# Performance work log

Hardware: AMD Instinct MI355X
Metric: run time of the kernel (lower is better)

Reference implementation:

```python
import jax, jax.numpy as jnp
import numpy as np

EMBED_DIM = 1024
SCALE = 1.0 / float(np.sqrt(EMBED_DIM))


def setup_inputs() -> dict:
    key = jax.random.key(0)
    ks = jax.random.split(key, 7)
    B, S, D = 4, 2048, EMBED_DIM
    init = 1.0 / np.sqrt(D)
    x = jax.random.normal(ks[0], (B, S, D), dtype=jnp.float32)
    Wq = jax.random.uniform(ks[1], (D, D), jnp.float32, -init, init)
    bq = jax.random.uniform(ks[2], (D,), jnp.float32, -init, init)
    Wk = jax.random.uniform(ks[3], (D, D), jnp.float32, -init, init)
    bk = jax.random.uniform(ks[4], (D,), jnp.float32, -init, init)
    Wv = jax.random.uniform(ks[5], (D, D), jnp.float32, -init, init)
    bv = jax.random.uniform(ks[6], (D,), jnp.float32, -init, init)
    return {"x": x, "Wq": Wq, "bq": bq, "Wk": Wk, "bk": bk, "Wv": Wv, "bv": bv}


def reference(x, Wq, bq, Wk, bk, Wv, bv):
    # Linear projections (torch Linear: x @ W.T + b; here W stored as [in, out])
    q = x @ Wq + bq  # [B, S, D]
    k = x @ Wk + bk
    v = x @ Wv + bv
    # Manual scaled dot-product attention (single head)
    scores = jnp.einsum("bsd,btd->bst", q, k) * SCALE  # [B, S, S]
    attn = jax.nn.softmax(scores, axis=-1)
    # Dropout is identity at inference (eval mode); p=0.1 at train time.
    return jnp.einsum("bst,btd->bsd", attn, v)
```

## Files before the change

### kernel.cpp

```cpp
#include <hip/hip_runtime.h>

#define MODE_QKV 0
#define MODE_S   1
#define MODE_PV  2

typedef __attribute__((ext_vector_type(8))) short short8;
typedef __attribute__((ext_vector_type(4))) float floatx4;

typedef const unsigned __attribute__((address_space(1)))* gp_t;
typedef unsigned __attribute__((address_space(3)))* lp_t;

__device__ __forceinline__ void async16(const void* g, void* l) {
  __builtin_amdgcn_global_load_lds((gp_t)g, (lp_t)l, 16, 0, 0);
}

__device__ __forceinline__ unsigned short f2bf(float f) {
  union { float f; unsigned u; } x; x.f = f;
  unsigned r = x.u + 0x7fffu + ((x.u >> 16) & 1u);
  return (unsigned short)(r >> 16);
}
__device__ __forceinline__ float bf2f(unsigned short h) {
  union { unsigned u; float f; } x; x.u = ((unsigned)h) << 16;
  return x.f;
}

union SmemU {
  struct { unsigned short A[2][4096]; unsigned short B[2][4096]; } st;
  unsigned short epi[128 * 136];
};

template<int MODE>
__global__ __launch_bounds__(256, 4)
void gemm_nt(const unsigned short* __restrict__ A,
             const unsigned short* __restrict__ Bmat,
             const float* __restrict__ b0, const float* __restrict__ b1,
             const float* __restrict__ b2,
             unsigned short* __restrict__ O0, unsigned short* __restrict__ O1,
             unsigned short* __restrict__ O2,
             float* __restrict__ Of, float* __restrict__ lsum,
             int M, int N, int K, long aZ, long bZ, long cZ, float scale)
{
  __shared__ SmemU smem;

  const int tid = threadIdx.x;
  const int wave = tid >> 6, lane = tid & 63;
  const int wm = wave >> 1, wn = wave & 1;
  const int quad = lane >> 4, l16 = lane & 15;

  const int gx = gridDim.x, gy = gridDim.y;
  int z, bm, bn;
  {
    int f = (blockIdx.z * gy + blockIdx.y) * gx + blockIdx.x;
    int T = gx * gy * (int)gridDim.z;
    int nsq = T >> 7;
    int xcd = f & 7, i = f >> 3;
    int sq = xcd * nsq + (i >> 4);
    int w = i & 15;
    int spz = (gx >> 2) * (gy >> 2);
    z = sq / spz;
    int sqr = sq - z * spz;
    int sqm = sqr / (gx >> 2), sqn = sqr - sqm * (gx >> 2);
    bm = (sqm * 4 + (w >> 2)) * 128;
    bn = (sqn * 4 + (w & 3)) * 128;
  }

  const unsigned short* Ap = (MODE == MODE_QKV) ? A : (A + (long)z * aZ);
  const unsigned short* Bp = Bmat + (long)z * bZ;

  floatx4 acc[4][4];
  #pragma unroll
  for (int i = 0; i < 4; i++)
    #pragma unroll
    for (int j = 0; j < 4; j++)
      acc[i][j] = (floatx4){0.f, 0.f, 0.f, 0.f};

  char* asb = (char*)&smem.st.A[0][0] + wave * 1024;
  char* bsb = (char*)&smem.st.B[0][0] + wave * 1024;

  for (int k0 = 0; k0 < K; k0 += 64) {
    #pragma unroll
    for (int p = 0; p < 2; p++) {
      #pragma unroll
      for (int h = 0; h < 2; h++) {
        int flat = tid + h * 256;
        int r = flat >> 2, c = (flat & 3) << 3;
        async16(Ap + (long)(bm + r) * K + k0 + p * 32 + c,
                asb + p * 8192 + h * 4096);
        async16(Bp + (long)(bn + r) * K + k0 + p * 32 + c,
                bsb + p * 8192 + h * 4096);
      }
    }
    __syncthreads();

    #pragma unroll
    for (int ks = 0; ks < 2; ks++) {
      short8 afr[4], bfr[4];
      #pragma unroll
      for (int i = 0; i < 4; i++)
        afr[i] = *(const short8*)&smem.st.A[ks][(wm * 64 + i * 16 + l16) * 32 + quad * 8];
      #pragma unroll
      for (int i = 0; i < 4; i++)
        bfr[i] = *(const short8*)&smem.st.B[ks][(wn * 64 + i * 16 + l16) * 32 + quad * 8];
      #pragma unroll
      for (int mi = 0; mi < 4; mi++)
        #pragma unroll
        for (int ni = 0; ni < 4; ni++)
          acc[mi][ni] = __builtin_amdgcn_mfma_f32_16x16x32_bf16(
              afr[mi], bfr[ni], acc[mi][ni], 0, 0, 0);
    }
    __syncthreads();
  }

  if (MODE == MODE_PV) {
    #pragma unroll
    for (int mi = 0; mi < 4; mi++) {
      int row0 = bm + wm * 64 + mi * 16 + quad * 4;
      float inv[4];
      #pragma unroll
      for (int r = 0; r < 4; r++)
        inv[r] = 1.0f / lsum[(long)z * M + row0 + r];
      #pragma unroll
      for (int ni = 0; ni < 4; ni++) {
        int col = bn + wn * 64 + ni * 16 + l16;
        #pragma unroll
        for (int r = 0; r < 4; r++)
          Of[(long)z * cZ + (long)(row0 + r) * N + col] = acc[mi][ni][r] * inv[r];
      }
    }
    return;
  }

  const bool vtrans = (MODE == MODE_QKV) && (z == 2);
  float bi[4];
  if (MODE == MODE_QKV) {
    const float* bias = (z == 0) ? b0 : ((z == 1) ? b1 : b2);
    #pragma unroll
    for (int ni = 0; ni < 4; ni++) bi[ni] = bias[bn + wn * 64 + ni * 16 + l16];
  }

  #pragma unroll
  for (int ni = 0; ni < 4; ni++) {
    int col = wn * 64 + ni * 16 + l16;
    float bb = (MODE == MODE_QKV) ? bi[ni] : 0.f;
    #pragma unroll
    for (int mi = 0; mi < 4; mi++) {
      int row0 = wm * 64 + mi * 16 + quad * 4;
      if (MODE == MODE_S) {
        #pragma unroll
        for (int r = 0; r < 4; r++)
          smem.epi[(row0 + r) * 136 + col] = f2bf(__expf(acc[mi][ni][r] * scale));
      } else if (!vtrans) {
        #pragma unroll
        for (int r = 0; r < 4; r++)
          smem.epi[(row0 + r) * 136 + col] = f2bf(acc[mi][ni][r] + bb);
      } else {
        #pragma unroll
        for (int r = 0; r < 4; r += 2) {
          unsigned lo = f2bf(acc[mi][ni][r] + bb);
          unsigned hi = f2bf(acc[mi][ni][r + 1] + bb);
          *(unsigned*)&smem.epi[col * 136 + row0 + r] = lo | (hi << 16);
        }
      }
    }
  }
  __syncthreads();

  #pragma unroll
  for (int i = 0; i < 8; i++) {
    int flat = i * 2048 + tid * 8;
    int rr = flat >> 7, cc = flat & 127;
    short8 vline = *(const short8*)&smem.epi[rr * 136 + cc];
    if (MODE == MODE_S) {
      union { short8 v; unsigned short u[8]; } t; t.v = vline;
      float s8 = 0.f;
      #pragma unroll
      for (int j = 0; j < 8; j++) s8 += bf2f(t.u[j]);
      s8 += __shfl_xor(s8, 1);
      s8 += __shfl_xor(s8, 2);
      s8 += __shfl_xor(s8, 4);
      s8 += __shfl_xor(s8, 8);
      if ((lane & 15) == 0) atomicAdd(&lsum[(long)z * M + bm + rr], s8);
      *(short8*)&O0[(long)z * cZ + (long)(bm + rr) * N + bn + cc] = vline;
    } else if (!vtrans) {
      unsigned short* O = (z == 0) ? O0 : O1;
      *(short8*)&O[(long)(bm + rr) * N + bn + cc] = vline;
    } else {
      int bb = bm >> 11, s0 = bm & 2047;
      *(short8*)&O2[(long)bb * (1024L * 2048) + (long)(bn + rr) * 2048 + s0 + cc] = vline;
    }
  }
}

__global__ __launch_bounds__(256)
void prep_kernel(const float* __restrict__ x, unsigned short* __restrict__ xb,
                 const float* __restrict__ W0, const float* __restrict__ W1,
                 const float* __restrict__ W2, unsigned short* __restrict__ Wt,
                 float* __restrict__ lsum) {
  int blk = blockIdx.x;
  if (blk < 4096) {
    long i = ((long)blk * 256 + threadIdx.x) * 8;
    float4 a = *(const float4*)(x + i);
    float4 b = *(const float4*)(x + i + 4);
    union { int4 v; unsigned short u[8]; } t;
    t.u[0] = f2bf(a.x); t.u[1] = f2bf(a.y); t.u[2] = f2bf(a.z); t.u[3] = f2bf(a.w);
    t.u[4] = f2bf(b.x); t.u[5] = f2bf(b.y); t.u[6] = f2bf(b.z); t.u[7] = f2bf(b.w);
    *(int4*)(xb + i) = t.v;
  } else if (blk < 7168) {
    __shared__ float tile[32][33];
    int tt = blk - 4096;
    int zz = tt >> 10, rem = tt & 1023;
    int kb = (rem >> 5) * 32, nb = (rem & 31) * 32;
    const float* W = (zz == 0) ? W0 : ((zz == 1) ? W1 : W2);
    unsigned short* O = Wt + (long)zz * 1024 * 1024;
    int t = threadIdx.x, tr = t >> 5, tc = t & 31;
    #pragma unroll
    for (int i = 0; i < 4; i++)
      tile[tr + i * 8][tc] = W[(long)(kb + tr + i * 8) * 1024 + nb + tc];
    __syncthreads();
    #pragma unroll
    for (int i = 0; i < 4; i++)
      O[(long)(nb + tr + i * 8) * 1024 + kb + tc] = f2bf(tile[tc][tr + i * 8]);
  } else {
    int i = (blk - 7168) * 256 + threadIdx.x;
    lsum[i] = 0.f;
  }
}

extern "C" void kernel_launch(void* const* d_in, const int* in_sizes, int n_in,
                              void* d_out, int out_size, void* d_ws, size_t ws_size,
                              hipStream_t stream) {
  const float* x  = (const float*)d_in[0];
  const float* Wq = (const float*)d_in[1];
  const float* bq = (const float*)d_in[2];
  const float* Wk = (const float*)d_in[3];
  const float* bk = (const float*)d_in[4];
  const float* Wv = (const float*)d_in[5];
  const float* bv = (const float*)d_in[6];
  float* out = (float*)d_out;

  const int B = 4, S = 2048, D = 1024;
  const int M = B * S;
  const float scale = 0.03125f;

  unsigned short* xb = (unsigned short*)d_out;
  unsigned short* Wt = xb + (size_t)M * D;
  unsigned short* q  = (unsigned short*)d_ws;
  unsigned short* k  = q + (size_t)M * D;
  unsigned short* vT = k + (size_t)M * D;
  unsigned short* P  = vT + (size_t)M * D;

  size_t need_full = ((size_t)3 * M * D + (size_t)B * S * S) * sizeof(unsigned short)
                   + (size_t)M * sizeof(float);
  const bool full = (ws_size >= need_full);
  float* lsum = full ? (float*)(P + (size_t)B * S * S)
                     : (float*)(P + (size_t)S * S);

  prep_kernel<<<7200, 256, 0, stream>>>(x, xb, Wq, Wk, Wv, Wt, lsum);

  gemm_nt<MODE_QKV><<<dim3(D / 128, M / 128, 3), 256, 0, stream>>>(
      xb, Wt, bq, bk, bv, q, k, vT, nullptr, nullptr,
      M, D, D, 0, (long)D * D, 0, 1.0f);

  if (full) {
    gemm_nt<MODE_S><<<dim3(S / 128, S / 128, B), 256, 0, stream>>>(
        q, k, nullptr, nullptr, nullptr, P, nullptr, nullptr, nullptr, lsum,
        S, S, D, (long)S * D, (long)S * D, (long)S * S, scale);
    gemm_nt<MODE_PV><<<dim3(D / 128, S / 128, B), 256, 0, stream>>>(
        P, vT, nullptr, nullptr, nullptr, nullptr, nullptr, nullptr, out, lsum,
        S, D, S, (long)S * S, (long)D * S, (long)S * D, 1.0f);
  } else {
    for (int b = 0; b < B; b++) {
      const unsigned short* qb = q + (size_t)b * S * D;
      const unsigned short* kb = k + (size_t)b * S * D;
      const unsigned short* vb = vT + (size_t)b * S * D;
      float* ob = out + (size_t)b * S * D;
      gemm_nt<MODE_S><<<dim3(S / 128, S / 128, 1), 256, 0, stream>>>(
          qb, kb, nullptr, nullptr, nullptr, P, nullptr, nullptr, nullptr,
          lsum + (size_t)b * S,
          S, S, D, 0, 0, 0, scale);
      gemm_nt<MODE_PV><<<dim3(D / 128, S / 128, 1), 256, 0, stream>>>(
          P, vb, nullptr, nullptr, nullptr, nullptr, nullptr, nullptr, ob,
          lsum + (size_t)b * S,
          S, D, S, 0, 0, 0, 1.0f);
    }
  }
}
```

Before: 236.0 us.

## Add 256x256-tile, 512-thread GEMM kernel for QKV and score stages

Adds a new gemm256 kernel with 256x256 output tiles, 8 waves, a swizzled LDS layout, async global-to-LDS double buffering staged in quarter steps interleaved with MFMA blocks, and an XCD-aware tile remapping. The QKV projection and the score (exp) GEMM now use it, while PV keeps the old 128-tile kernel. Larger tiles raise operand reuse and cut global traffic per FLOP, but at one block per CU they lower occupancy and use 128KB of LDS. The block remapping assumes grid sizes divisible by 128 blocks and by 4x4 squares.

Result: slower. 242.5 us (+2.7%).

```diff
diff --git a/kernel.cpp b/kernel.cpp
--- a/kernel.cpp
+++ b/kernel.cpp
@@ -23,6 +23,253 @@
   union { unsigned u; float f; } x; x.u = ((unsigned)h) << 16;
   return x.f;
 }
+
+
+__device__ __forceinline__ void stage_half(const unsigned short* gp, long rowbase,
+                                           int ldk, int kb, char* region,
+                                           int wave, int lane) {
+  const int rs = lane >> 3;
+  const int kc = ((lane & 7) ^ rs) << 3;
+  #pragma unroll
+  for (int h = 0; h < 2; h++) {
+    const int rr = (h * 8 + wave) * 8 + rs;
+    async16(gp + (rowbase + rr) * (long)ldk + kb + kc,
+            region + (h * 8 + wave) * 1024);
+  }
+}
+
+__device__ __forceinline__ short8 frag(const char* region, int hr, int ks, int quad) {
+  return *(const short8*)(region + hr * 128 + ((((ks << 2) | quad) ^ (hr & 7)) << 4));
+}
+
+#define MFMA_QUAD(MH, NH)                                                    \
+  do {                                                                       \
+    _Pragma("unroll")                                                        \
+    for (int mi_ = 0; mi_ < 4; mi_++) {                                      \
+      _Pragma("unroll")                                                      \
+      for (int jj_ = 0; jj_ < 2; jj_++) {                                    \
+        _Pragma("unroll")                                                    \
+        for (int ks_ = 0; ks_ < 2; ks_++) {                                  \
+          acc[MH][mi_][NH][jj_] = __builtin_amdgcn_mfma_f32_16x16x32_bf16(   \
+              a[mi_][ks_], b[NH][jj_][ks_], acc[MH][mi_][NH][jj_], 0, 0, 0); \
+        }                                                                    \
+      }                                                                      \
+    }                                                                        \
+  } while (0)
+
+template<int MODE>
+__global__ __launch_bounds__(512, 1)
+void gemm256(const unsigned short* __restrict__ A,
+             const unsigned short* __restrict__ Bmat,
+             const float* __restrict__ b0, const float* __restrict__ b1,
+             const float* __restrict__ b2,
+             unsigned short* __restrict__ O0, unsigned short* __restrict__ O1,
+             unsigned short* __restrict__ O2, float* __restrict__ lsum,
+             int M, int N, int K, long aZ, long bZ, long cZ, float scale)
+{
+  __shared__ __attribute__((aligned(128))) char lds[131072];
+
+  const int tid = threadIdx.x;
+  const int wave = tid >> 6, lane = tid & 63;
+  const int wm = wave >> 2, wn = wave & 3;
+  const int quad = lane >> 4, l16 = lane & 15;
+
+  const int gx = gridDim.x, gy = gridDim.y;
+  int z, bm, bn;
+  {
+    int f = (blockIdx.z * gy + blockIdx.y) * gx + blockIdx.x;
+    int T = gx * gy * (int)gridDim.z;
+    int nsq = T >> 7;
+    int xcd = f & 7, i = f >> 3;
+    int sq = xcd * nsq + (i >> 4);
+    int w = i & 15;
+    int spz = (gx >> 2) * (gy >> 2);
+    z = sq / spz;
+    int sqr = sq - z * spz;
+    int sqm = sqr / (gx >> 2), sqn = sqr - sqm * (gx >> 2);
+    bm = (sqm * 4 + (w >> 2)) * 256;
+    bn = (sqn * 4 + (w & 3)) * 256;
+  }
+
+  const unsigned short* Ap = (MODE == MODE_QKV) ? A : (A + (long)z * aZ);
+  const unsigned short* Bp = Bmat + (long)z * bZ;
+
+  const int NT = K >> 6;
+
+  stage_half(Ap, bm,       K, 0,  lds +     0, wave, lane);
+  stage_half(Bp, bn,       K, 0,  lds + 32768, wave, lane);
+  stage_half(Bp, bn + 128, K, 0,  lds + 49152, wave, lane);
+  stage_half(Ap, bm + 128, K, 0,  lds + 16384, wave, lane);
+  stage_half(Ap, bm,       K, 64, lds + 65536 +     0, wave, lane);
+  stage_half(Bp, bn,       K, 64, lds + 65536 + 32768, wave, lane);
+  stage_half(Bp, bn + 128, K, 64, lds + 65536 + 49152, wave, lane);
+  asm volatile("s_waitcnt vmcnt(6)" ::: "memory");
+  __builtin_amdgcn_s_barrier();
+
+  floatx4 acc[2][4][2][2];
+  #pragma unroll
+  for (int p = 0; p < 2; p++)
+    #pragma unroll
+    for (int q2 = 0; q2 < 4; q2++)
+      #pragma unroll
+      for (int r = 0; r < 2; r++)
+        #pragma unroll
+        for (int s = 0; s < 2; s++)
+          acc[p][q2][r][s] = (floatx4){0.f, 0.f, 0.f, 0.f};
+
+  short8 a[4][2];
+  short8 b[2][2][2];
+
+  for (int j = 0; j < NT; j++) {
+    char* bufc = lds + ((j & 1) << 16);
+    char* bufn = lds + (((j + 1) & 1) << 16);
+    const bool lp = (j + 2 >= NT);
+    const int kn  = (j + 1) << 6;
+    const int kn2 = (j + 2) << 6;
+
+    #pragma unroll
+    for (int mi = 0; mi < 4; mi++)
+      #pragma unroll
+      for (int ks = 0; ks < 2; ks++)
+        a[mi][ks] = frag(bufc, wm * 64 + mi * 16 + l16, ks, quad);
+    #pragma unroll
+    for (int jj = 0; jj < 2; jj++)
+      #pragma unroll
+      for (int ks = 0; ks < 2; ks++)
+        b[0][jj][ks] = frag(bufc + 32768, wn * 32 + jj * 16 + l16, ks, quad);
+    if (j + 1 < NT)
+      stage_half(Ap, bm + 128, K, kn, bufn + 16384, wave, lane);
+    __builtin_amdgcn_s_barrier();
+    asm volatile("s_waitcnt lgkmcnt(0)" ::: "memory");
+    __builtin_amdgcn_sched_barrier(0);
+    __builtin_amdgcn_s_setprio(1);
+    MFMA_QUAD(0, 0);
+    __builtin_amdgcn_s_setprio(0);
+    __builtin_amdgcn_s_barrier();
+
+    #pragma unroll
+    for (int jj = 0; jj < 2; jj++)
+      #pragma unroll
+      for (int ks = 0; ks < 2; ks++)
+        b[1][jj][ks] = frag(bufc + 49152, wn * 32 + jj * 16 + l16, ks, quad);
+    if (!lp)
+      stage_half(Ap, bm, K, kn2, bufc, wave, lane);
+    __builtin_amdgcn_s_barrier();
+    asm volatile("s_waitcnt lgkmcnt(0)" ::: "memory");
+    __builtin_amdgcn_sched_barrier(0);
+    __builtin_amdgcn_s_setprio(1);
+    MFMA_QUAD(0, 1);
+    __builtin_amdgcn_s_setprio(0);
+    __builtin_amdgcn_s_barrier();
+
+    #pragma unroll
+    for (int mi = 0; mi < 4; mi++)
+      #pragma unroll
+      for (int ks = 0; ks < 2; ks++)
+        a[mi][ks] = frag(bufc + 16384, wm * 64 + mi * 16 + l16, ks, quad);
+    if (!lp)
+      stage_half(Bp, bn, K, kn2, bufc + 32768, wave, lane);
+    __builtin_amdgcn_s_barrier();
+    asm volatile("s_waitcnt lgkmcnt(0)" ::: "memory");
+    __builtin_amdgcn_sched_barrier(0);
+    __builtin_amdgcn_s_setprio(1);
+    MFMA_QUAD(1, 0);
+    __builtin_amdgcn_s_setprio(0);
+    __builtin_amdgcn_s_barrier();
+
+    if (!lp) {
+      stage_half(Bp, bn + 128, K, kn2, bufc + 49152, wave, lane);
+      asm volatile("s_waitcnt vmcnt(6)" ::: "memory");
+    } else {
+      asm volatile("s_waitcnt vmcnt(0)" ::: "memory");
+    }
+    __builtin_amdgcn_s_barrier();
+    __builtin_amdgcn_s_setprio(1);
+    MFMA_QUAD(1, 1);
+    __builtin_amdgcn_s_setprio(0);
+    __builtin_amdgcn_s_barrier();
+  }
+
+  const bool vtrans = (MODE == MODE_QKV) && (z == 2);
+  float bi[2][2];
+  if (MODE == MODE_QKV) {
+    const float* bias = (z == 0) ? b0 : ((z == 1) ? b1 : b2);
+    #pragma unroll
+    for (int nh = 0; nh < 2; nh++)
+      #pragma unroll
+      for (int jj = 0; jj < 2; jj++)
+        bi[nh][jj] = bias[bn + nh * 128 + wn * 32 + jj * 16 + l16];
+  }
+
+  unsigned short* epi = (unsigned short*)lds;
+  #pragma unroll
+  for (int mh = 0; mh < 2; mh++) {
+    #pragma unroll
+    for (int mi = 0; mi < 4; mi++) {
+      const int r0 = wm * 64 + mi * 16 + quad * 4;
+      #pragma unroll
+      for (int nh = 0; nh < 2; nh++)
+        #pragma unroll
+        for (int jj = 0; jj < 2; jj++) {
+          const int col = nh * 128 + wn * 32 + jj * 16 + l16;
+          if (MODE == MODE_S) {
+            #pragma unroll
+            for (int r = 0; r < 4; r++)
+              epi[(r0 + r) * 264 + col] = f2bf(__expf(acc[mh][mi][nh][jj][r] * scale));
+          } else if (!vtrans) {
+            #pragma unroll
+            for (int r = 0; r < 4; r++)
+              epi[(r0 + r) * 264 + col] = f2bf(acc[mh][mi][nh][jj][r] + bi[nh][jj]);
+          } else {
+            #pragma unroll
+            for (int r = 0; r < 4; r += 2) {
+              unsigned lo = f2bf(acc[mh][mi][nh][jj][r] + bi[nh][jj]);
+              unsigned hi = f2bf(acc[mh][mi][nh][jj][r + 1] + bi[nh][jj]);
+              *(unsigned*)&epi[col * 136 + r0 + r] = lo | (hi << 16);
+            }
+          }
+        }
+    }
+    __syncthreads();
+
+    if (!vtrans) {
+      #pragma unroll
+      for (int it = 0; it < 8; it++) {
+        int flat = it * 4096 + tid * 8;
+        int rr = flat >> 8, cc = flat & 255;
+        short8 vline = *(const short8*)&epi[rr * 264 + cc];
+        long grow = bm + mh * 128 + rr;
+        if (MODE == MODE_S) {
+          union { short8 v; unsigned short u[8]; } t; t.v = vline;
+          float s8 = 0.f;
+          #pragma unroll
+          for (int jq = 0; jq < 8; jq++) s8 += bf2f(t.u[jq]);
+          s8 += __shfl_xor(s8, 1);
+          s8 += __shfl_xor(s8, 2);
+          s8 += __shfl_xor(s8, 4);
+          s8 += __shfl_xor(s8, 8);
+          s8 += __shfl_xor(s8, 16);
+          if ((lane & 31) == 0) atomicAdd(&lsum[(long)z * M + grow], s8);
+          *(short8*)&O0[(long)z * cZ + grow * N + bn + cc] = vline;
+        } else {
+          unsigned short* O = (z == 0) ? O0 : O1;
+          *(short8*)&O[grow * N + bn + cc] = vline;
+        }
+      }
+    } else {
+      int bb = bm >> 11, s0 = bm & 2047;
+      #pragma unroll
+      for (int it = 0; it < 8; it++) {
+        int flat = it * 4096 + tid * 8;
+        int dd = flat >> 7, ss = flat & 127;
+        short8 vline = *(const short8*)&epi[dd * 136 + ss];
+        *(short8*)&O2[(long)bb * (1024L * 2048) + (long)(bn + dd) * 2048 + s0 + mh * 128 + ss] = vline;
+      }
+    }
+    if (mh == 0) __syncthreads();
+  }
+}
+
 
 union SmemU {
   struct { unsigned short A[2][4096]; unsigned short B[2][4096]; } st;
@@ -257,13 +504,13 @@
 
   prep_kernel<<<7200, 256, 0, stream>>>(x, xb, Wq, Wk, Wv, Wt, lsum);
 
-  gemm_nt<MODE_QKV><<<dim3(D / 128, M / 128, 3), 256, 0, stream>>>(
-      xb, Wt, bq, bk, bv, q, k, vT, nullptr, nullptr,
+  gemm256<MODE_QKV><<<dim3(D / 256, M / 256, 3), 512, 0, stream>>>(
+      xb, Wt, bq, bk, bv, q, k, vT, nullptr,
       M, D, D, 0, (long)D * D, 0, 1.0f);
 
   if (full) {
-    gemm_nt<MODE_S><<<dim3(S / 128, S / 128, B), 256, 0, stream>>>(
-        q, k, nullptr, nullptr, nullptr, P, nullptr, nullptr, nullptr, lsum,
+    gemm256<MODE_S><<<dim3(S / 256, S / 256, B), 512, 0, stream>>>(
+        q, k, nullptr, nullptr, nullptr, P, nullptr, nullptr, lsum,
         S, S, D, (long)S * D, (long)S * D, (long)S * S, scale);
     gemm_nt<MODE_PV><<<dim3(D / 128, S / 128, B), 256, 0, stream>>>(
         P, vT, nullptr, nullptr, nullptr, nullptr, nullptr, nullptr, out, lsum,
```
